# Performance work log

Hardware: AMD Instinct MI355X
Metric: run time of the kernel (lower is better)

The kernel has to match this reference:

```python
import jax, jax.numpy as jnp
import numpy as np

N, E, D, H, G, O = 50000, 800000, 128, 256, 128, 10
BN_EPS = 1e-5
SLOPE = 0.2  # LeakyReLU negative slope


def setup_inputs() -> dict:
    keys = iter(jax.random.split(jax.random.key(0), 64))

    def rn(shape, scale=0.05):
        return jax.random.normal(next(keys), shape, jnp.float32) * scale

    inp = {
        "x": jax.random.normal(next(keys), (N, D), jnp.float32),
        "edge_index": jax.random.randint(next(keys), (2, E), 0, N),
        "edge_attr": jax.random.normal(next(keys), (E, 3), jnp.float32),
        "batch": jnp.sort(jax.random.randint(next(keys), (N,), 0, G)),
    }
    for i, din in zip((1, 2, 3), (D, H, H)):
        inp[f"We{i}"] = rn((3, din))
        inp[f"be{i}"] = jnp.zeros((din,), jnp.float32)
        inp[f"W{i}1"] = rn((din, H))
        inp[f"b{i}1"] = jnp.zeros((H,), jnp.float32)
        inp[f"g{i}"] = jnp.ones((H,), jnp.float32)
        inp[f"bt{i}"] = jnp.zeros((H,), jnp.float32)
        inp[f"mu{i}"] = jnp.zeros((H,), jnp.float32)
        inp[f"var{i}"] = jnp.ones((H,), jnp.float32)
        inp[f"W{i}2"] = rn((H, H))
        inp[f"b{i}2"] = jnp.zeros((H,), jnp.float32)
    for name, shape in (("Wm1", (3 * H, 200)), ("Wm2", (200, 200)), ("Wm3", (200, 200)), ("Wm4", (200, O))):
        inp[name] = rn(shape)
        inp["b" + name[1:]] = jnp.zeros((shape[1],), jnp.float32)
    return inp


def _leaky(v):
    return jax.nn.leaky_relu(v, SLOPE)


def _gine(x, src, dst, ea, We, be, W1, b1, g, bt, mu, var, W2, b2):
    # message: ReLU(x_j + lin_edge(edge_attr)); aggregate: scatter-sum to dst
    msg = jax.nn.relu(x[src] + ea @ We + be)          # [E, din]
    agg = jax.ops.segment_sum(msg, dst, num_segments=N)  # [N, din]
    h = x + agg                                       # (1+eps)*x_i + agg, eps=0
    h = h @ W1 + b1
    h = g * (h - mu) * jax.lax.rsqrt(var + BN_EPS) + bt  # BatchNorm1d (eval)
    h = _leaky(h)
    return _leaky(h @ W2 + b2)


def reference(x, edge_index, edge_attr, batch,
              We1, be1, W11, b11, g1, bt1, mu1, var1, W12, b12,
              We2, be2, W21, b21, g2, bt2, mu2, var2, W22, b22,
              We3, be3, W31, b31, g3, bt3, mu3, var3, W32, b32,
              Wm1, bm1, Wm2, bm2, Wm3, bm3, Wm4, bm4):
    src, dst = edge_index[0], edge_index[1]
    x1 = _gine(x, src, dst, edge_attr, We1, be1, W11, b11, g1, bt1, mu1, var1, W12, b12)
    x2 = _gine(x1, src, dst, edge_attr, We2, be2, W21, b21, g2, bt2, mu2, var2, W22, b22)
    x3 = _gine(x2, src, dst, edge_attr, We3, be3, W31, b31, g3, bt3, mu3, var3, W32, b32)
    p1 = jax.ops.segment_sum(x1, batch, num_segments=G)  # global_add_pool
    p2 = jax.ops.segment_sum(x2, batch, num_segments=G)
    p3 = jax.ops.segment_sum(x3, batch, num_segments=G)
    h = jnp.concatenate((p1, p2, p3), axis=1)            # [G, 3H]
    # MLP (dropout is identity at inference); note doubled LeakyReLU in source
    h = _leaky(_leaky(h @ Wm1 + bm1))
    h = _leaky(_leaky(h @ Wm2 + bm2))
    h = _leaky(_leaky(h @ Wm3 + bm3))
    return h @ Wm4 + bm4                                 # [G, O]
```

## Files before the change

kernel.cpp:

```cpp
#include <hip/hip_runtime.h>
#include <hip/hip_fp16.h>

#define LRELU(v) ((v) >= 0.f ? (v) : 0.2f * (v))
#define DLRELU(v) ((v) >= 0.f ? (v) : 0.04f * (v))

constexpr int Nn = 50000;
constexpr int Ee = 800000;
constexpr int Hh = 256;
constexpr int Gg = 128;
constexpr int Oo = 10;

typedef __attribute__((ext_vector_type(8))) short short8;
typedef __attribute__((ext_vector_type(4))) float f32x4;
typedef __attribute__((ext_vector_type(4))) unsigned int uv4;
typedef __attribute__((ext_vector_type(2))) unsigned int uv2;
typedef __attribute__((ext_vector_type(4))) unsigned short us4;

__device__ inline unsigned short f2h(float f) {
  __half h = __float2half_rn(f);
  return *reinterpret_cast<unsigned short*>(&h);
}
__device__ inline float h2f(unsigned short u) {
  __half h = *reinterpret_cast<__half*>(&u);
  return __half2float(h);
}
__device__ inline __half2 u2h2(unsigned int u) {
  return *reinterpret_cast<__half2*>(&u);
}
__device__ inline unsigned int h22u(__half2 h) {
  return *reinterpret_cast<unsigned int*>(&h);
}
__device__ inline __half2 hmax2(__half2 a, __half2 b) {
  __half2 r;
  asm volatile("v_pk_max_f16 %0, %1, %2" : "=v"(r) : "v"(a), "v"(b));
  return r;
}
__device__ inline unsigned short f2bf(float f) {
  union { float f; unsigned int i; } v; v.f = f;
  unsigned int i = v.i;
  return (unsigned short)((i + 0x7FFFu + ((i >> 16) & 1u)) >> 16);
}

typedef __attribute__((address_space(1))) const unsigned int gu32;
typedef __attribute__((address_space(3))) unsigned int lu32;
__device__ inline void gload_lds16(const void* g, void* l) {
  __builtin_amdgcn_global_load_lds((gu32*)g, (lu32*)l, 16, 0, 0);
}

__global__ __launch_bounds__(256) void hist_kernel(
    const int* __restrict__ dst, int* __restrict__ deg)
{
  const int e = blockIdx.x * 256 + threadIdx.x;
  if (e < Ee) atomicAdd(&deg[dst[e]], 1);
}

__global__ __launch_bounds__(1024) void scan1_kernel(
    const int* __restrict__ deg, int* __restrict__ bsum)
{
  const int i = blockIdx.x * 1024 + threadIdx.x;
  int v = (i < Nn) ? deg[i] : 0;
  #pragma unroll
  for (int o = 32; o; o >>= 1) v += __shfl_xor(v, o, 64);
  __shared__ int ws[16];
  const int wid = threadIdx.x >> 6, lane = threadIdx.x & 63;
  if (lane == 0) ws[wid] = v;
  __syncthreads();
  if (threadIdx.x == 0) {
    int s = 0;
    #pragma unroll
    for (int k = 0; k < 16; k++) s += ws[k];
    bsum[blockIdx.x] = s;
  }
}

__global__ __launch_bounds__(64) void scan2_kernel(
    const int* __restrict__ bsum, int* __restrict__ boff, int* __restrict__ row_ptr, int nb)
{
  if (threadIdx.x == 0) {
    int s = 0;
    for (int b = 0; b < nb; b++) { boff[b] = s; s += bsum[b]; }
    row_ptr[Nn] = s;
  }
}

__global__ __launch_bounds__(1024) void scan3_kernel(
    const int* __restrict__ deg, const int* __restrict__ boff,
    int* __restrict__ row_ptr, int* __restrict__ cursor)
{
  const int i = blockIdx.x * 1024 + threadIdx.x;
  const int wid = threadIdx.x >> 6, lane = threadIdx.x & 63;
  const int v = (i < Nn) ? deg[i] : 0;
  int inc = v;
  #pragma unroll
  for (int o = 1; o < 64; o <<= 1) {
    const int u = __shfl_up(inc, o, 64);
    if (lane >= o) inc += u;
  }
  __shared__ int ws[16];
  if (lane == 63) ws[wid] = inc;
  __syncthreads();
  if (wid == 0 && lane < 16) {
    int s = ws[lane];
    #pragma unroll
    for (int o = 1; o < 16; o <<= 1) {
      const int u = __shfl_up(s, o, 64);
      if (lane >= o) s += u;
    }
    ws[lane] = s;
  }
  __syncthreads();
  const int woff = (wid == 0) ? 0 : ws[wid - 1];
  const int excl = boff[blockIdx.x] + woff + inc - v;
  if (i < Nn) { row_ptr[i] = excl; cursor[i] = excl; }
}

__global__ __launch_bounds__(256) void fill_kernel(
    const int* __restrict__ src, const int* __restrict__ dst,
    const float* __restrict__ ea, int* __restrict__ cursor,
    uv4* __restrict__ edges)
{
  const int e = blockIdx.x * 256 + threadIdx.x;
  if (e >= Ee) return;
  const int pos = atomicAdd(&cursor[dst[e]], 1);
  uv4 r;
  r.x = (unsigned)src[e];
  r.y = h22u(__float2half2_rn(ea[3 * e + 0]));
  r.z = h22u(__float2half2_rn(ea[3 * e + 1]));
  r.w = h22u(__float2half2_rn(ea[3 * e + 2]));
  edges[pos] = r;
}

__global__ __launch_bounds__(256) void f2h_kernel(
    const float* __restrict__ in, unsigned short* __restrict__ out, int n4)
{
  const int i = blockIdx.x * 256 + threadIdx.x;
  if (i >= n4) return;
  const float4 v = *reinterpret_cast<const float4*>(in + (size_t)i * 4);
  us4 o; o.x = f2h(v.x); o.y = f2h(v.y); o.z = f2h(v.z); o.w = f2h(v.w);
  *reinterpret_cast<us4*>(out + (size_t)i * 4) = o;
}

__global__ __launch_bounds__(256) void f2bf_kernel(
    const float* __restrict__ in, unsigned short* __restrict__ out, int n4)
{
  const int i = blockIdx.x * 256 + threadIdx.x;
  if (i >= n4) return;
  const float4 v = *reinterpret_cast<const float4*>(in + (size_t)i * 4);
  us4 o; o.x = f2bf(v.x); o.y = f2bf(v.y); o.z = f2bf(v.z); o.w = f2bf(v.w);
  *reinterpret_cast<us4*>(out + (size_t)i * 4) = o;
}

__global__ __launch_bounds__(256) void wt_kernel(
    const float* __restrict__ W, unsigned short* __restrict__ Bt, int K)
{
  const int g = blockIdx.x * 256 + threadIdx.x;
  if (g >= 256 * K) return;
  const int c = g & 255, k = g >> 8;
  Bt[(size_t)c * K + k] = f2h(W[(size_t)k * 256 + c]);
}

__global__ __launch_bounds__(256) void headwt_kernel(
    const float* __restrict__ W, unsigned short* __restrict__ Bt,
    int K, int M, int Kpad)
{
  const int g = blockIdx.x * 256 + threadIdx.x;
  if (g >= 256 * Kpad) return;
  const int c = g / Kpad, k = g % Kpad;
  Bt[(size_t)c * Kpad + k] = (c < M && k < K) ? f2bf(W[(size_t)k * M + c]) : (unsigned short)0;
}

template<int DIN>
__global__ __launch_bounds__(256) void agg_gather(
    const unsigned short* __restrict__ x, const uv4* __restrict__ edges,
    const float* __restrict__ We, const float* __restrict__ be,
    const int* __restrict__ row_ptr, unsigned short* __restrict__ S)
{
  constexpr int FPL = DIN / 64;
  constexpr int H2  = FPL / 2;
  constexpr int SH  = (DIN == 256) ? 8 : 7;
  const int wv   = threadIdx.x >> 6;
  const int lane = threadIdx.x & 63;
  const int n = blockIdx.x * 4 + wv;
  if (n >= Nn) return;
  const int fo = lane * FPL;

  const __half2 zero2 = __float2half2_rn(0.f);
  __half2 w0h[H2], w1h[H2], w2h[H2], bbh[H2], acc[H2];
  #pragma unroll
  for (int j = 0; j < H2; j++) {
    w0h[j] = __halves2half2(__float2half_rn(We[0 * DIN + fo + 2 * j]),
                            __float2half_rn(We[0 * DIN + fo + 2 * j + 1]));
    w1h[j] = __halves2half2(__float2half_rn(We[1 * DIN + fo + 2 * j]),
                            __float2half_rn(We[1 * DIN + fo + 2 * j + 1]));
    w2h[j] = __halves2half2(__float2half_rn(We[2 * DIN + fo + 2 * j]),
                            __float2half_rn(We[2 * DIN + fo + 2 * j + 1]));
    bbh[j] = __halves2half2(__float2half_rn(be[fo + 2 * j]),
                            __float2half_rn(be[fo + 2 * j + 1]));
    acc[j] = zero2;
  }

  const int beg = row_ptr[n], end = row_ptr[n + 1];
  int i = beg;

  for (; i + 4 <= end; i += 4) {
    uv4 e[4];
    #pragma unroll
    for (int q = 0; q < 4; q++) e[q] = __builtin_nontemporal_load(edges + i + q);
    __half2 xv[4][H2];
    #pragma unroll
    for (int q = 0; q < 4; q++) {
      const unsigned o = (e[q].x << SH) + fo;
      if constexpr (H2 == 2) {
        const uv2 r = *reinterpret_cast<const uv2*>(x + o);
        xv[q][0] = u2h2(r.x); xv[q][1] = u2h2(r.y);
      } else {
        xv[q][0] = u2h2(*reinterpret_cast<const unsigned int*>(x + o));
      }
    }
    #pragma unroll
    for (int q = 0; q < 4; q++) {
      const __half2 a0 = u2h2(e[q].y), a1 = u2h2(e[q].z), a2 = u2h2(e[q].w);
      #pragma unroll
      for (int j = 0; j < H2; j++) {
        __half2 m = __hadd2(xv[q][j], bbh[j]);
        m = __hfma2(a2, w2h[j], m);
        m = __hfma2(a1, w1h[j], m);
        m = __hfma2(a0, w0h[j], m);
        acc[j] = __hadd2(acc[j], hmax2(m, zero2));
      }
    }
  }
  for (; i < end; i++) {
    const uv4 e0 = __builtin_nontemporal_load(edges + i);
    const unsigned o0 = (e0.x << SH) + fo;
    __half2 xv0[H2];
    if constexpr (H2 == 2) {
      const uv2 r0 = *reinterpret_cast<const uv2*>(x + o0);
      xv0[0] = u2h2(r0.x); xv0[1] = u2h2(r0.y);
    } else {
      xv0[0] = u2h2(*reinterpret_cast<const unsigned int*>(x + o0));
    }
    const __half2 a00 = u2h2(e0.y), a01 = u2h2(e0.z), a02 = u2h2(e0.w);
    #pragma unroll
    for (int j = 0; j < H2; j++) {
      __half2 m0 = __hadd2(xv0[j], bbh[j]);
      m0 = __hfma2(a02, w2h[j], m0);
      m0 = __hfma2(a01, w1h[j], m0);
      m0 = __hfma2(a00, w0h[j], m0);
      acc[j] = __hadd2(acc[j], hmax2(m0, zero2));
    }
  }

  const unsigned on = ((unsigned)n << SH) + fo;
  if constexpr (H2 == 2) {
    const uv2 rs = *reinterpret_cast<const uv2*>(x + on);
    const float2 s0 = __half22float2(u2h2(rs.x)), s1 = __half22float2(u2h2(rs.y));
    const float2 f0 = __half22float2(acc[0]), f1 = __half22float2(acc[1]);
    uv2 o;
    o.x = (unsigned)f2h(s0.x + f0.x) | ((unsigned)f2h(s0.y + f0.y) << 16);
    o.y = (unsigned)f2h(s1.x + f1.x) | ((unsigned)f2h(s1.y + f1.y) << 16);
    __builtin_nontemporal_store(o, reinterpret_cast<uv2*>(S + on));
  } else {
    const float2 s0 = __half22float2(u2h2(*reinterpret_cast<const unsigned int*>(x + on)));
    const float2 f0 = __half22float2(acc[0]);
    const unsigned o = (unsigned)f2h(s0.x + f0.x) | ((unsigned)f2h(s0.y + f0.y) << 16);
    __builtin_nontemporal_store(o, reinterpret_cast<unsigned int*>(S + on));
  }
}

template<int K, bool DOBN>
__global__ __launch_bounds__(256) void gemm_mfma(
    const unsigned short* __restrict__ A, const unsigned short* __restrict__ Bt,
    const float* __restrict__ bias,
    const float* __restrict__ gamma, const float* __restrict__ beta,
    const float* __restrict__ mu, const float* __restrict__ var,
    unsigned short* __restrict__ C)
{
  __shared__ __align__(16) unsigned short lA[128 * 64];
  __shared__ __align__(16) unsigned short lB[128 * 64];
  const int t = threadIdx.x;
  const int lane = t & 63, wid = t >> 6;
  const int wrow = wid >> 1, wcol = wid & 1;
  const int l15 = lane & 15, hi = lane >> 4;
  const int n0 = blockIdx.y * 128;
  const int c0 = blockIdx.x * 128;
  const int srow = lane >> 3;
  const int sslot = lane & 7;

  f32x4 acc[4][4] = {};

  for (int k0 = 0; k0 < K; k0 += 64) {
    #pragma unroll
    for (int c = 0; c < 4; c++) {
      const int chunk = wid * 4 + c;
      const int row = chunk * 8 + srow;
      const int scol = (sslot ^ (row & 7)) * 8;
      const int gr = min(n0 + row, Nn - 1);
      gload_lds16(A + (size_t)gr * K + k0 + scol, (char*)lA + chunk * 1024);
      const int cb = c0 + row;
      gload_lds16(Bt + (size_t)cb * K + k0 + scol, (char*)lB + chunk * 1024);
    }
    __syncthreads();
    #pragma unroll
    for (int kk = 0; kk < 2; kk++) {
      short8 av[4], bv[4];
      #pragma unroll
      for (int rf = 0; rf < 4; rf++) {
        const int ar = wrow * 64 + rf * 16 + l15;
        av[rf] = *reinterpret_cast<const short8*>(
            (const char*)lA + ar * 128 + (((kk * 4 + hi) ^ (ar & 7)) << 4));
      }
      #pragma unroll
      for (int cf = 0; cf < 4; cf++) {
        const int br = wcol * 64 + cf * 16 + l15;
        bv[cf] = *reinterpret_cast<const short8*>(
            (const char*)lB + br * 128 + (((kk * 4 + hi) ^ (br & 7)) << 4));
      }
      #pragma unroll
      for (int rf = 0; rf < 4; rf++)
        #pragma unroll
        for (int cf = 0; cf < 4; cf++)
          acc[rf][cf] = __builtin_amdgcn_mfma_f32_16x16x32_f16(av[rf], bv[cf], acc[rf][cf], 0, 0, 0);
    }
    __syncthreads();
  }

  #pragma unroll
  for (int cf = 0; cf < 4; cf++) {
    const int col = c0 + wcol * 64 + cf * 16 + l15;
    const float bs = bias[col];
    float gm = 0.f, bt2 = 0.f, mm = 0.f, iv = 0.f;
    if constexpr (DOBN) {
      gm = gamma[col]; bt2 = beta[col]; mm = mu[col];
      iv = rsqrtf(var[col] + 1e-5f);
    }
    #pragma unroll
    for (int rf = 0; rf < 4; rf++) {
      #pragma unroll
      for (int rg = 0; rg < 4; rg++) {
        const int row = n0 + wrow * 64 + rf * 16 + hi * 4 + rg;
        if (row >= Nn) continue;
        float v = acc[rf][cf][rg] + bs;
        if constexpr (DOBN) v = gm * (v - mm) * iv + bt2;
        v = LRELU(v);
        C[(size_t)row * 256 + col] = f2h(v);
      }
    }
  }
}

__global__ __launch_bounds__(256) void pool_kernel(
    const unsigned short* __restrict__ xl, const int* __restrict__ batch,
    float* __restrict__ pooled, int layer)
{
  constexpr int NPB = 16;
  const int n0 = blockIdx.x * NPB;
  const int c  = threadIdx.x;
  if (n0 >= Nn) return;
  float acc = 0.f;
  int curb = batch[n0];
  for (int i = 0; i < NPB; i++) {
    const int n = n0 + i;
    if (n >= Nn) break;
    const int b = batch[n];
    if (b != curb) {
      atomicAdd(pooled + (size_t)curb * 768 + layer * 256 + c, acc);
      acc = 0.f;
      curb = b;
    }
    acc += h2f(xl[(size_t)n * 256 + c]);
  }
  atomicAdd(pooled + (size_t)curb * 768 + layer * 256 + c, acc);
}

__global__ __launch_bounds__(256) void head_fused(
    const unsigned short* __restrict__ P,
    const unsigned short* __restrict__ B1t,
    const unsigned short* __restrict__ B2t,
    const unsigned short* __restrict__ B3t,
    const unsigned short* __restrict__ B4t,
    const float* __restrict__ b1, const float* __restrict__ b2,
    const float* __restrict__ b3, const float* __restrict__ b4,
    float* __restrict__ out)
{
  __shared__ __align__(16) unsigned short act[32 * 256];
  const int t = threadIdx.x, lane = t & 63, wid = t >> 6;
  const int l15 = lane & 15, hi = lane >> 4;
  const int r0 = blockIdx.x * 32;

  f32x4 acc[2][4];

  #pragma unroll
  for (int rf = 0; rf < 2; rf++)
    #pragma unroll
    for (int cf = 0; cf < 4; cf++) acc[rf][cf] = (f32x4){0.f, 0.f, 0.f, 0.f};
  #pragma unroll 2
  for (int ks = 0; ks < 24; ks++) {
    short8 bv[4], av[2];
    #pragma unroll
    for (int cf = 0; cf < 4; cf++) {
      const int c = wid * 64 + cf * 16 + l15;
      bv[cf] = *reinterpret_cast<const short8*>(B1t + (size_t)c * 768 + ks * 32 + hi * 8);
    }
    #pragma unroll
    for (int rf = 0; rf < 2; rf++)
      av[rf] = *reinterpret_cast<const short8*>(
          P + (size_t)(r0 + rf * 16 + l15) * 768 + ks * 32 + hi * 8);
    #pragma unroll
    for (int rf = 0; rf < 2; rf++)
      #pragma unroll
      for (int cf = 0; cf < 4; cf++)
        acc[rf][cf] = __builtin_amdgcn_mfma_f32_16x16x32_bf16(av[rf], bv[cf], acc[rf][cf], 0, 0, 0);
  }
  #pragma unroll
  for (int cf = 0; cf < 4; cf++) {
    const int c = wid * 64 + cf * 16 + l15;
    const float bs = (c < 200) ? b1[c] : 0.f;
    const int slot0 = c >> 3;
    #pragma unroll
    for (int rf = 0; rf < 2; rf++)
      #pragma unroll
      for (int rg = 0; rg < 4; rg++) {
        const int row = rf * 16 + hi * 4 + rg;
        const float v = DLRELU(acc[rf][cf][rg] + bs);
        act[row * 256 + ((slot0 ^ (row & 7)) << 3) + (c & 7)] = f2bf(v);
      }
  }
  __syncthreads();

  #pragma unroll
  for (int L = 0; L < 2; L++) {
    const unsigned short* B = (L == 0) ? B2t : B3t;
    const float* bias = (L == 0) ? b2 : b3;
    #pragma unroll
    for (int rf = 0; rf < 2; rf++)
      #pragma unroll
      for (int cf = 0; cf < 4; cf++) acc[rf][cf] = (f32x4){0.f, 0.f, 0.f, 0.f};
    #pragma unroll
    for (int ks = 0; ks < 8; ks++) {
      short8 bv[4], av[2];
      #pragma unroll
      for (int cf = 0; cf < 4; cf++) {
        const int c = wid * 64 + cf * 16 + l15;
        bv[cf] = *reinterpret_cast<const short8*>(B + (size_t)c * 256 + ks * 32 + hi * 8);
      }
      #pragma unroll
      for (int rf = 0; rf < 2; rf++) {
        const int row = rf * 16 + l15;
        const int slot = ks * 4 + hi;
        av[rf] = *reinterpret_cast<const short8*>(
            act + row * 256 + ((slot ^ (row & 7)) << 3));
      }
      #pragma unroll
      for (int rf = 0; rf < 2; rf++)
        #pragma unroll
        for (int cf = 0; cf < 4; cf++)
          acc[rf][cf] = __builtin_amdgcn_mfma_f32_16x16x32_bf16(av[rf], bv[cf], acc[rf][cf], 0, 0, 0);
    }
    __syncthreads();
    #pragma unroll
    for (int cf = 0; cf < 4; cf++) {
      const int c = wid * 64 + cf * 16 + l15;
      const float bs = (c < 200) ? bias[c] : 0.f;
      const int slot0 = c >> 3;
      #pragma unroll
      for (int rf = 0; rf < 2; rf++)
        #pragma unroll
        for (int rg = 0; rg < 4; rg++) {
          const int row = rf * 16 + hi * 4 + rg;
          const float v = DLRELU(acc[rf][cf][rg] + bs);
          act[row * 256 + ((slot0 ^ (row & 7)) << 3) + (c & 7)] = f2bf(v);
        }
    }
    __syncthreads();
  }

  if (wid == 0) {
    f32x4 a4[2] = {};
    #pragma unroll
    for (int ks = 0; ks < 8; ks++) {
      short8 av[2];
      const short8 bv = *reinterpret_cast<const short8*>(
          B4t + (size_t)l15 * 256 + ks * 32 + hi * 8);
      #pragma unroll
      for (int rf = 0; rf < 2; rf++) {
        const int row = rf * 16 + l15;
        const int slot = ks * 4 + hi;
        av[rf] = *reinterpret_cast<const short8*>(
            act + row * 256 + ((slot ^ (row & 7)) << 3));
      }
      #pragma unroll
      for (int rf = 0; rf < 2; rf++)
        a4[rf] = __builtin_amdgcn_mfma_f32_16x16x32_bf16(av[rf], bv, a4[rf], 0, 0, 0);
    }
    if (l15 < Oo) {
      const float bs = b4[l15];
      #pragma unroll
      for (int rf = 0; rf < 2; rf++)
        #pragma unroll
        for (int rg = 0; rg < 4; rg++) {
          const int row = r0 + rf * 16 + hi * 4 + rg;
          out[(size_t)row * Oo + l15] = a4[rf][rg] + bs;
        }
    }
  }
}

extern "C" void kernel_launch(void* const* d_in, const int* in_sizes, int n_in,
                              void* d_out, int out_size, void* d_ws, size_t ws_size,
                              hipStream_t stream)
{
  const float* x     = (const float*)d_in[0];
  const int*   ei    = (const int*)d_in[1];
  const float* ea    = (const float*)d_in[2];
  const int*   batch = (const int*)d_in[3];
  const int* src = ei;
  const int* dst = ei + Ee;

  const float *We[3], *be_[3], *W1[3], *b1[3], *g_[3], *bt_[3], *mu_[3], *var_[3], *W2[3], *b2[3];
  for (int l = 0; l < 3; l++) {
    const int base = 4 + l * 10;
    We[l]  = (const float*)d_in[base + 0];
    be_[l] = (const float*)d_in[base + 1];
    W1[l]  = (const float*)d_in[base + 2];
    b1[l]  = (const float*)d_in[base + 3];
    g_[l]  = (const float*)d_in[base + 4];
    bt_[l] = (const float*)d_in[base + 5];
    mu_[l] = (const float*)d_in[base + 6];
    var_[l]= (const float*)d_in[base + 7];
    W2[l]  = (const float*)d_in[base + 8];
    b2[l]  = (const float*)d_in[base + 9];
  }
  const float *Wm[4], *bm[4];
  for (int i = 0; i < 4; i++) {
    Wm[i] = (const float*)d_in[34 + 2 * i];
    bm[i] = (const float*)d_in[35 + 2 * i];
  }

  int* deg     = (int*)d_ws;
  int* cursor  = deg + Nn;
  int* row_ptr = cursor + Nn;
  int* bsum    = row_ptr + Nn + 4;
  int* boff    = bsum + 64;
  uv4* edges   = (uv4*)(boff + 64);
  unsigned short* x0h  = (unsigned short*)(edges + Ee);
  unsigned short* Wt11 = x0h + (size_t)Nn * 128;
  unsigned short* Wt12 = Wt11 + 32768;
  unsigned short* Wt21 = Wt12 + 65536;
  unsigned short* Wt22 = Wt21 + 65536;
  unsigned short* Wt31 = Wt22 + 65536;
  unsigned short* Wt32 = Wt31 + 65536;
  unsigned short* HW1t = Wt32 + 65536;
  unsigned short* HW2t = HW1t + 256 * 768;
  unsigned short* HW3t = HW2t + 65536;
  unsigned short* HW4t = HW3t + 65536;
  unsigned short* S    = HW4t + 65536;
  unsigned short* Y    = S  + (size_t)Nn * Hh;
  unsigned short* XB0  = Y  + (size_t)Nn * Hh;
  unsigned short* XB1  = XB0 + (size_t)Nn * Hh;
  unsigned short* Pbf  = XB1 + (size_t)Nn * Hh;
  float* pooled = (float*)(Pbf + (size_t)Gg * 768);
  float* outf  = (float*)d_out;

  const dim3 gemmGrid(2, (Nn + 127) / 128);
  const int  poolGrid = (Nn + 15) / 16;
  const int  aggGrid  = (Nn + 3) / 4;
  const int  eGrid    = (Ee + 255) / 256;
  const int  sGrid    = (Nn + 1023) / 1024;

  hipMemsetAsync(deg, 0, Nn * sizeof(int), stream);
  hipMemsetAsync(pooled, 0, (size_t)Gg * 768 * sizeof(float), stream);

  hist_kernel<<<eGrid, 256, 0, stream>>>(dst, deg);
  scan1_kernel<<<sGrid, 1024, 0, stream>>>(deg, bsum);
  scan2_kernel<<<1, 64, 0, stream>>>(bsum, boff, row_ptr, sGrid);
  scan3_kernel<<<sGrid, 1024, 0, stream>>>(deg, boff, row_ptr, cursor);
  fill_kernel<<<eGrid, 256, 0, stream>>>(src, dst, ea, cursor, edges);

  f2h_kernel<<<(Nn * 128 / 4 + 255) / 256, 256, 0, stream>>>(x, x0h, Nn * 128 / 4);
  wt_kernel<<<(256 * 128 + 255) / 256, 256, 0, stream>>>(W1[0], Wt11, 128);
  wt_kernel<<<(256 * 256 + 255) / 256, 256, 0, stream>>>(W2[0], Wt12, 256);
  wt_kernel<<<(256 * 256 + 255) / 256, 256, 0, stream>>>(W1[1], Wt21, 256);
  wt_kernel<<<(256 * 256 + 255) / 256, 256, 0, stream>>>(W2[1], Wt22, 256);
  wt_kernel<<<(256 * 256 + 255) / 256, 256, 0, stream>>>(W1[2], Wt31, 256);
  wt_kernel<<<(256 * 256 + 255) / 256, 256, 0, stream>>>(W2[2], Wt32, 256);
  headwt_kernel<<<(256 * 768 + 255) / 256, 256, 0, stream>>>(Wm[0], HW1t, 768, 200, 768);
  headwt_kernel<<<(256 * 256 + 255) / 256, 256, 0, stream>>>(Wm[1], HW2t, 200, 200, 256);
  headwt_kernel<<<(256 * 256 + 255) / 256, 256, 0, stream>>>(Wm[2], HW3t, 200, 200, 256);
  headwt_kernel<<<(256 * 256 + 255) / 256, 256, 0, stream>>>(Wm[3], HW4t, 200, 10, 256);

  agg_gather<128><<<aggGrid, 256, 0, stream>>>(x0h, edges, We[0], be_[0], row_ptr, S);
  gemm_mfma<128, true><<<gemmGrid, 256, 0, stream>>>(
      S, Wt11, b1[0], g_[0], bt_[0], mu_[0], var_[0], Y);
  gemm_mfma<256, false><<<gemmGrid, 256, 0, stream>>>(
      Y, Wt12, b2[0], nullptr, nullptr, nullptr, nullptr, XB0);
  pool_kernel<<<poolGrid, 256, 0, stream>>>(XB0, batch, pooled, 0);

  agg_gather<256><<<aggGrid, 256, 0, stream>>>(XB0, edges, We[1], be_[1], row_ptr, S);
  gemm_mfma<256, true><<<gemmGrid, 256, 0, stream>>>(
      S, Wt21, b1[1], g_[1], bt_[1], mu_[1], var_[1], Y);
  gemm_mfma<256, false><<<gemmGrid, 256, 0, stream>>>(
      Y, Wt22, b2[1], nullptr, nullptr, nullptr, nullptr, XB1);
  pool_kernel<<<poolGrid, 256, 0, stream>>>(XB1, batch, pooled, 1);

  agg_gather<256><<<aggGrid, 256, 0, stream>>>(XB1, edges, We[2], be_[2], row_ptr, S);
  gemm_mfma<256, true><<<gemmGrid, 256, 0, stream>>>(
      S, Wt31, b1[2], g_[2], bt_[2], mu_[2], var_[2], Y);
  gemm_mfma<256, false><<<gemmGrid, 256, 0, stream>>>(
      Y, Wt32, b2[2], nullptr, nullptr, nullptr, nullptr, XB0);
  pool_kernel<<<poolGrid, 256, 0, stream>>>(XB0, batch, pooled, 2);

  f2bf_kernel<<<(Gg * 768 / 4 + 255) / 256, 256, 0, stream>>>(pooled, Pbf, Gg * 768 / 4);
  head_fused<<<4, 256, 0, stream>>>(Pbf, HW1t, HW2t, HW3t, HW4t,
                                    bm[0], bm[1], bm[2], bm[3], outf);
}
```

Before: 653.2 us.

## Widen GEMM tile to full 256 columns and batch weight transposes into one launch

The node GEMMs now use 512-thread blocks, each computing a 128x256 tile that covers the whole output width. Each A row tile is loaded into LDS once instead of twice across two column blocks. LDS for B doubles to 32 KB per block, which may reduce occupancy. Separately, the ten weight-transpose/convert launches are merged into one kernel driven by a job table, cutting launch overhead.

```diff
diff --git a/kernel.cpp b/kernel.cpp
--- a/kernel.cpp
+++ b/kernel.cpp
@@ -150,23 +150,28 @@
   *reinterpret_cast<us4*>(out + (size_t)i * 4) = o;
 }
 
-__global__ __launch_bounds__(256) void wt_kernel(
-    const float* __restrict__ W, unsigned short* __restrict__ Bt, int K)
-{
-  const int g = blockIdx.x * 256 + threadIdx.x;
-  if (g >= 256 * K) return;
-  const int c = g & 255, k = g >> 8;
-  Bt[(size_t)c * K + k] = f2h(W[(size_t)k * 256 + c]);
-}
-
-__global__ __launch_bounds__(256) void headwt_kernel(
-    const float* __restrict__ W, unsigned short* __restrict__ Bt,
-    int K, int M, int Kpad)
-{
-  const int g = blockIdx.x * 256 + threadIdx.x;
+struct WtJobs {
+  const float* src[10];
+  unsigned short* dst[10];
+  int K[10], M[10], Kpad[10], isbf[10], blk0[11];
+};
+
+__global__ __launch_bounds__(256) void wtall_kernel(WtJobs J)
+{
+  int j = 0;
+  #pragma unroll
+  for (int q = 1; q < 10; q++) if ((int)blockIdx.x >= J.blk0[q]) j = q;
+  const int g = ((int)blockIdx.x - J.blk0[j]) * 256 + threadIdx.x;
+  const int Kpad = J.Kpad[j];
   if (g >= 256 * Kpad) return;
   const int c = g / Kpad, k = g % Kpad;
-  Bt[(size_t)c * Kpad + k] = (c < M && k < K) ? f2bf(W[(size_t)k * M + c]) : (unsigned short)0;
+  const int K = J.K[j], M = J.M[j];
+  unsigned short o = 0;
+  if (c < M && k < K) {
+    const float w = J.src[j][(size_t)k * M + c];
+    o = J.isbf[j] ? f2bf(w) : f2h(w);
+  }
+  J.dst[j][(size_t)c * Kpad + k] = o;
 }
 
 template<int DIN>
@@ -269,7 +274,7 @@
 }
 
 template<int K, bool DOBN>
-__global__ __launch_bounds__(256) void gemm_mfma(
+__global__ __launch_bounds__(512) void gemm_mfma(
     const unsigned short* __restrict__ A, const unsigned short* __restrict__ Bt,
     const float* __restrict__ bias,
     const float* __restrict__ gamma, const float* __restrict__ beta,
@@ -277,13 +282,12 @@
     unsigned short* __restrict__ C)
 {
   __shared__ __align__(16) unsigned short lA[128 * 64];
-  __shared__ __align__(16) unsigned short lB[128 * 64];
+  __shared__ __align__(16) unsigned short lB[256 * 64];
   const int t = threadIdx.x;
   const int lane = t & 63, wid = t >> 6;
-  const int wrow = wid >> 1, wcol = wid & 1;
+  const int wrow = wid >> 2, wcol = wid & 3;
   const int l15 = lane & 15, hi = lane >> 4;
   const int n0 = blockIdx.y * 128;
-  const int c0 = blockIdx.x * 128;
   const int srow = lane >> 3;
   const int sslot = lane & 7;
 
@@ -291,14 +295,19 @@
 
   for (int k0 = 0; k0 < K; k0 += 64) {
     #pragma unroll
-    for (int c = 0; c < 4; c++) {
-      const int chunk = wid * 4 + c;
-      const int row = chunk * 8 + srow;
-      const int scol = (sslot ^ (row & 7)) * 8;
-      const int gr = min(n0 + row, Nn - 1);
-      gload_lds16(A + (size_t)gr * K + k0 + scol, (char*)lA + chunk * 1024);
-      const int cb = c0 + row;
-      gload_lds16(Bt + (size_t)cb * K + k0 + scol, (char*)lB + chunk * 1024);
+    for (int c = 0; c < 6; c++) {
+      const int chunk = wid * 6 + c;
+      if (chunk < 16) {
+        const int row = chunk * 8 + srow;
+        const int scol = (sslot ^ (row & 7)) * 8;
+        const int gr = min(n0 + row, Nn - 1);
+        gload_lds16(A + (size_t)gr * K + k0 + scol, (char*)lA + chunk * 1024);
+      } else {
+        const int bchunk = chunk - 16;
+        const int row = bchunk * 8 + srow;
+        const int scol = (sslot ^ (row & 7)) * 8;
+        gload_lds16(Bt + (size_t)row * K + k0 + scol, (char*)lB + bchunk * 1024);
+      }
     }
     __syncthreads();
     #pragma unroll
@@ -327,7 +336,7 @@
 
   #pragma unroll
   for (int cf = 0; cf < 4; cf++) {
-    const int col = c0 + wcol * 64 + cf * 16 + l15;
+    const int col = wcol * 64 + cf * 16 + l15;
     const float bs = bias[col];
     float gm = 0.f, bt2 = 0.f, mm = 0.f, iv = 0.f;
     if constexpr (DOBN) {
@@ -562,7 +571,7 @@
   float* pooled = (float*)(Pbf + (size_t)Gg * 768);
   float* outf  = (float*)d_out;
 
-  const dim3 gemmGrid(2, (Nn + 127) / 128);
+  const dim3 gemmGrid(1, (Nn + 127) / 128);
   const int  poolGrid = (Nn + 15) / 16;
   const int  aggGrid  = (Nn + 3) / 4;
   const int  eGrid    = (Ee + 255) / 256;
@@ -578,35 +587,43 @@
   fill_kernel<<<eGrid, 256, 0, stream>>>(src, dst, ea, cursor, edges);
 
   f2h_kernel<<<(Nn * 128 / 4 + 255) / 256, 256, 0, stream>>>(x, x0h, Nn * 128 / 4);
-  wt_kernel<<<(256 * 128 + 255) / 256, 256, 0, stream>>>(W1[0], Wt11, 128);
-  wt_kernel<<<(256 * 256 + 255) / 256, 256, 0, stream>>>(W2[0], Wt12, 256);
-  wt_kernel<<<(256 * 256 + 255) / 256, 256, 0, stream>>>(W1[1], Wt21, 256);
-  wt_kernel<<<(256 * 256 + 255) / 256, 256, 0, stream>>>(W2[1], Wt22, 256);
-  wt_kernel<<<(256 * 256 + 255) / 256, 256, 0, stream>>>(W1[2], Wt31, 256);
-  wt_kernel<<<(256 * 256 + 255) / 256, 256, 0, stream>>>(W2[2], Wt32, 256);
-  headwt_kernel<<<(256 * 768 + 255) / 256, 256, 0, stream>>>(Wm[0], HW1t, 768, 200, 768);
-  headwt_kernel<<<(256 * 256 + 255) / 256, 256, 0, stream>>>(Wm[1], HW2t, 200, 200, 256);
-  headwt_kernel<<<(256 * 256 + 255) / 256, 256, 0, stream>>>(Wm[2], HW3t, 200, 200, 256);
-  headwt_kernel<<<(256 * 256 + 255) / 256, 256, 0, stream>>>(Wm[3], HW4t, 200, 10, 256);
+  {
+    WtJobs J;
+    const float* s[10] = {W1[0], W2[0], W1[1], W2[1], W1[2], W2[2], Wm[0], Wm[1], Wm[2], Wm[3]};
+    unsigned short* d[10] = {Wt11, Wt12, Wt21, Wt22, Wt31, Wt32, HW1t, HW2t, HW3t, HW4t};
+    const int Ks[10]   = {128, 256, 256, 256, 256, 256, 768, 200, 200, 200};
+    const int Ms[10]   = {256, 256, 256, 256, 256, 256, 200, 200, 200, 10};
+    const int Kp[10]   = {128, 256, 256, 256, 256, 256, 768, 256, 256, 256};
+    const int bf[10]   = {0, 0, 0, 0, 0, 0, 1, 1, 1, 1};
+    int blk = 0;
+    for (int q = 0; q < 10; q++) {
+      J.src[q] = s[q]; J.dst[q] = d[q];
+      J.K[q] = Ks[q]; J.M[q] = Ms[q]; J.Kpad[q] = Kp[q]; J.isbf[q] = bf[q];
+      J.blk0[q] = blk;
+      blk += (256 * Kp[q] + 255) / 256;
+    }
+    J.blk0[10] = blk;
+    wtall_kernel<<<blk, 256, 0, stream>>>(J);
+  }
 
   agg_gather<128><<<aggGrid, 256, 0, stream>>>(x0h, edges, We[0], be_[0], row_ptr, S);
-  gemm_mfma<128, true><<<gemmGrid, 256, 0, stream>>>(
+  gemm_mfma<128, true><<<gemmGrid, 512, 0, stream>>>(
       S, Wt11, b1[0], g_[0], bt_[0], mu_[0], var_[0], Y);
-  gemm_mfma<256, false><<<gemmGrid, 256, 0, stream>>>(
+  gemm_mfma<256, false><<<gemmGrid, 512, 0, stream>>>(
       Y, Wt12, b2[0], nullptr, nullptr, nullptr, nullptr, XB0);
   pool_kernel<<<poolGrid, 256, 0, stream>>>(XB0, batch, pooled, 0);
 
   agg_gather<256><<<aggGrid, 256, 0, stream>>>(XB0, edges, We[1], be_[1], row_ptr, S);
-  gemm_mfma<256, true><<<gemmGrid, 256, 0, stream>>>(
+  gemm_mfma<256, true><<<gemmGrid, 512, 0, stream>>>(
       S, Wt21, b1[1], g_[1], bt_[1], mu_[1], var_[1], Y);
-  gemm_mfma<256, false><<<gemmGrid, 256, 0, stream>>>(
+  gemm_mfma<256, false><<<gemmGrid, 512, 0, stream>>>(
       Y, Wt22, b2[1], nullptr, nullptr, nullptr, nullptr, XB1);
   pool_kernel<<<poolGrid, 256, 0, stream>>>(XB1, batch, pooled, 1);
 
   agg_gather<256><<<aggGrid, 256, 0, stream>>>(XB1, edges, We[2], be_[2], row_ptr, S);
-  gemm_mfma<256, true><<<gemmGrid, 256, 0, stream>>>(
+  gemm_mfma<256, true><<<gemmGrid, 512, 0, stream>>>(
       S, Wt31, b1[2], g_[2], bt_[2], mu_[2], var_[2], Y);
-  gemm_mfma<256, false><<<gemmGrid, 256, 0, stream>>>(
+  gemm_mfma<256, false><<<gemmGrid, 512, 0, stream>>>(
       Y, Wt32, b2[2], nullptr, nullptr, nullptr, nullptr, XB0);
   pool_kernel<<<poolGrid, 256, 0, stream>>>(XB0, batch, pooled, 2);
 
```

Measured after the change: 621.4 us. -4.9%, faster.
